# Kernel optimization log

Measured on AMD Instinct MI355X. Metric: run time of the kernel, lower is better.

## Reference

```python
import jax, jax.numpy as jnp
import numpy as np

V_MIN = -10.0
V_MAX = 10.0
NUM_ATOMS = 51
DISCOUNT = 0.99
BS = 524288


def setup_inputs() -> dict:
    key = jax.random.key(0)
    k1, k2, k3 = jax.random.split(key, 3)
    reward = jax.random.normal(k1, (BS, 1), dtype=jnp.float32)
    probs = jax.random.uniform(k2, (BS, NUM_ATOMS), dtype=jnp.float32)
    probs = probs / jnp.sum(probs, axis=-1, keepdims=True)  # valid distribution
    not_done = jnp.round(jax.random.uniform(k3, (BS, 1), dtype=jnp.float32))
    return {"reward": reward, "probs": probs, "not_done": not_done}


def reference(reward, probs, not_done):
    bs = probs.shape[0]
    atom_delta = (V_MAX - V_MIN) / (NUM_ATOMS - 1)
    atom_values = V_MIN + atom_delta * jnp.arange(NUM_ATOMS, dtype=jnp.float32)  # [A]
    # Bellman-shifted atom positions, clipped to support
    new_atom_values = reward + DISCOUNT * not_done * atom_values[None, :]  # [bs, A]
    new_atom_values = jnp.clip(new_atom_values, V_MIN, V_MAX)
    b = (new_atom_values - V_MIN) / atom_delta  # fractional atom index
    l = jnp.floor(b)
    u = jnp.ceil(b)
    d_m_l = (u + (l == u).astype(probs.dtype) - b) * probs
    d_m_u = (b - l) * probs
    li = l.astype(jnp.int32)
    ui = u.astype(jnp.int32)
    rows = jnp.arange(bs, dtype=jnp.int32)[:, None]  # [bs,1] broadcasts over atoms
    new_probs = (
        jnp.zeros_like(probs)
        .at[rows, li].add(d_m_l)
        .at[rows, ui].add(d_m_u)
    )
    return new_probs
```

## Files before the change

### kernel.cpp

```cpp
#include <hip/hip_runtime.h>


#define NUM_ATOMS 51
#define RPB 64
#define TILE (RPB * NUM_ATOMS)
#define NV4 (TILE / 4)

__global__ __launch_bounds__(RPB, 3) void catproj_kernel(
    const float* __restrict__ reward,
    const float* __restrict__ probs,
    const float* __restrict__ not_done,
    float* __restrict__ out)
{
    __shared__ float lds[TILE];

    const int tid = threadIdx.x;
    const int row = blockIdx.x * RPB + tid;
    const int base = blockIdx.x * TILE;

    const float r  = reward[row];
    const float nd = not_done[row];

    const float4* __restrict__ p4 = (const float4*)(probs + base);
    float4* __restrict__ l4 = (float4*)lds;
#pragma unroll
    for (int k = 0; k < 12; ++k) {
        const int i4 = k * RPB + tid;
        l4[i4] = p4[i4];
    }
    if (tid < NV4 - 12 * RPB)
        l4[12 * RPB + tid] = p4[12 * RPB + tid];
    __syncthreads();

    float* __restrict__ myrow = lds + tid * NUM_ATOMS;
    float p[NUM_ATOMS];
#pragma unroll
    for (int a = 0; a < NUM_ATOMS; ++a) p[a] = myrow[a];

#pragma unroll
    for (int a = 0; a < NUM_ATOMS; ++a) myrow[a] = 0.0f;

    const float c     = 0.99f * nd;
    const float base2 = fmaf(-25.f, c, fmaf(2.5f, r, 25.f));
    float curf = floorf(fminf(fmaxf(base2, 0.f), 50.f));
    float* dst = myrow + (int)curf;
    float accL = 0.f, accU = 0.f;
#pragma unroll
    for (int a = 0; a < NUM_ATOMS; ++a) {
        float b = fmaf(c, (float)a, base2);
        b = fminf(fmaxf(b, 0.f), 50.f);
        const float lf = floorf(b);
        const float pa = p[a];
        const float mu = (b - lf) * pa;
        const float ml = pa - mu;
        if (lf != curf) {
            *dst = accL;
            ++dst;
            accL = accU;
            accU = 0.f;
            curf = lf;
        }
        accL += ml;
        accU += mu;
    }
    *dst = accL;
    if (curf < 50.f) dst[1] = accU;
    __syncthreads();

    const float4* __restrict__ s4 = (const float4*)lds;
    float4* __restrict__ o4 = (float4*)(out + base);
#pragma unroll
    for (int k = 0; k < 12; ++k) {
        const int i4 = k * RPB + tid;
        o4[i4] = s4[i4];
    }
    if (tid < NV4 - 12 * RPB)
        o4[12 * RPB + tid] = s4[12 * RPB + tid];
}

extern "C" void kernel_launch(void* const* d_in, const int* in_sizes, int n_in,
                              void* d_out, int out_size, void* d_ws, size_t ws_size,
                              hipStream_t stream) {
    const float* reward   = (const float*)d_in[0];
    const float* probs    = (const float*)d_in[1];
    const float* not_done = (const float*)d_in[2];
    float* out = (float*)d_out;

    const int bs = in_sizes[0];
    const int grid = bs / RPB;
    catproj_kernel<<<grid, RPB, 0, stream>>>(reward, probs, not_done, out);
}
```

Before: 197.4 us.

## Split each row across four lanes with serialized LDS accumulation

Each row is now handled by four lanes, each projecting a 13-atom segment, instead of one thread walking all 51 atoms. Blocks grow to 256 threads (four waves of 16 rows each), and each wave stages its own quarter of the tile in LDS. Segments add their partial sums into the shared row, and the boundary writes are serialized across segments to avoid races. This cuts per-thread register pressure and the serial dependency chain, which should raise occupancy, at the cost of extra barriers, read-modify-write LDS traffic, and an explicit zeroing pass.

```diff
diff --git a/kernel.cpp b/kernel.cpp
--- a/kernel.cpp
+++ b/kernel.cpp
@@ -2,59 +2,73 @@
 
 
 #define NUM_ATOMS 51
-#define RPB 64
-#define TILE (RPB * NUM_ATOMS)
-#define NV4 (TILE / 4)
+#define ROWS_PER_WAVE 16
+#define WAVES_PER_BLOCK 4
+#define ROWS_PER_BLOCK (ROWS_PER_WAVE * WAVES_PER_BLOCK)
+#define TILE_FLOATS (ROWS_PER_BLOCK * NUM_ATOMS)
+#define QUARTER_FLOATS (ROWS_PER_WAVE * NUM_ATOMS)
+#define QUARTER_V4 (QUARTER_FLOATS / 4)
 
-__global__ __launch_bounds__(RPB, 3) void catproj_kernel(
+__global__ __launch_bounds__(256, 8) void catproj_kernel(
     const float* __restrict__ reward,
     const float* __restrict__ probs,
     const float* __restrict__ not_done,
     float* __restrict__ out)
 {
-    __shared__ float lds[TILE];
+    __shared__ __align__(16) float lds[TILE_FLOATS];
 
-    const int tid = threadIdx.x;
-    const int row = blockIdx.x * RPB + tid;
-    const int base = blockIdx.x * TILE;
+    const int tid  = threadIdx.x;
+    const int wave = tid >> 6;
+    const int lane = tid & 63;
+    const int qrow = lane >> 2;
+    const int seg  = lane & 3;
+
+    const int row   = blockIdx.x * ROWS_PER_BLOCK + wave * ROWS_PER_WAVE + qrow;
+    const int gbase = blockIdx.x * TILE_FLOATS + wave * QUARTER_FLOATS;
+
+    float* __restrict__ q = lds + wave * QUARTER_FLOATS;
+
+    const float4* __restrict__ g4 = (const float4*)(probs + gbase);
+    float4* __restrict__ q4 = (float4*)q;
+#pragma unroll
+    for (int k = 0; k < 3; ++k) q4[k * 64 + lane] = g4[k * 64 + lane];
+    if (lane < QUARTER_V4 - 192) q4[192 + lane] = g4[192 + lane];
 
     const float r  = reward[row];
     const float nd = not_done[row];
-
-    const float4* __restrict__ p4 = (const float4*)(probs + base);
-    float4* __restrict__ l4 = (float4*)lds;
-#pragma unroll
-    for (int k = 0; k < 12; ++k) {
-        const int i4 = k * RPB + tid;
-        l4[i4] = p4[i4];
-    }
-    if (tid < NV4 - 12 * RPB)
-        l4[12 * RPB + tid] = p4[12 * RPB + tid];
     __syncthreads();
 
-    float* __restrict__ myrow = lds + tid * NUM_ATOMS;
-    float p[NUM_ATOMS];
+    float* __restrict__ myrow = q + qrow * NUM_ATOMS;
+    const int a0 = seg * 13;
+    float p[13];
 #pragma unroll
-    for (int a = 0; a < NUM_ATOMS; ++a) p[a] = myrow[a];
+    for (int i = 0; i < 12; ++i) p[i] = myrow[a0 + i];
+    p[12] = (seg < 3) ? myrow[a0 + 12] : 0.0f;
+    __syncthreads();
 
+    const float4 z4 = make_float4(0.f, 0.f, 0.f, 0.f);
 #pragma unroll
-    for (int a = 0; a < NUM_ATOMS; ++a) myrow[a] = 0.0f;
+    for (int k = 0; k < 3; ++k) q4[k * 64 + lane] = z4;
+    if (lane < QUARTER_V4 - 192) q4[192 + lane] = z4;
+    __syncthreads();
 
     const float c     = 0.99f * nd;
     const float base2 = fmaf(-25.f, c, fmaf(2.5f, r, 25.f));
-    float curf = floorf(fminf(fmaxf(base2, 0.f), 50.f));
+    const float b0    = fminf(fmaxf(fmaf(c, (float)a0, base2), 0.f), 50.f);
+    float curf = floorf(b0);
     float* dst = myrow + (int)curf;
     float accL = 0.f, accU = 0.f;
 #pragma unroll
-    for (int a = 0; a < NUM_ATOMS; ++a) {
+    for (int i = 0; i < 13; ++i) {
+        const int a = a0 + i;
         float b = fmaf(c, (float)a, base2);
         b = fminf(fmaxf(b, 0.f), 50.f);
         const float lf = floorf(b);
-        const float pa = p[a];
+        const float pa = p[i];
         const float mu = (b - lf) * pa;
         const float ml = pa - mu;
         if (lf != curf) {
-            *dst = accL;
+            *dst += accL;
             ++dst;
             accL = accU;
             accU = 0.f;
@@ -63,19 +77,22 @@
         accL += ml;
         accU += mu;
     }
-    *dst = accL;
-    if (curf < 50.f) dst[1] = accU;
+
+    asm volatile("" ::: "memory");
+#pragma unroll
+    for (int s = 0; s < 4; ++s) {
+        if (seg == s) {
+            dst[0] += accL;
+            if (curf < 50.f) dst[1] += accU;
+        }
+        asm volatile("" ::: "memory");
+    }
     __syncthreads();
 
-    const float4* __restrict__ s4 = (const float4*)lds;
-    float4* __restrict__ o4 = (float4*)(out + base);
+    float4* __restrict__ o4 = (float4*)(out + gbase);
 #pragma unroll
-    for (int k = 0; k < 12; ++k) {
-        const int i4 = k * RPB + tid;
-        o4[i4] = s4[i4];
-    }
-    if (tid < NV4 - 12 * RPB)
-        o4[12 * RPB + tid] = s4[12 * RPB + tid];
+    for (int k = 0; k < 3; ++k) o4[k * 64 + lane] = q4[k * 64 + lane];
+    if (lane < QUARTER_V4 - 192) o4[192 + lane] = q4[192 + lane];
 }
 
 extern "C" void kernel_launch(void* const* d_in, const int* in_sizes, int n_in,
@@ -87,6 +104,6 @@
     float* out = (float*)d_out;
 
     const int bs = in_sizes[0];
-    const int grid = bs / RPB;
-    catproj_kernel<<<grid, RPB, 0, stream>>>(reward, probs, not_done, out);
+    const int grid = bs / ROWS_PER_BLOCK;
+    catproj_kernel<<<grid, 256, 0, stream>>>(reward, probs, not_done, out);
 }
```

Measured after the change: 197.1 us. About the same (-0.1%).
